# Performance work log

Measured on AMD Instinct MI355X. Metric: run time of the kernel, lower is better.

## Reference

```python
import jax, jax.numpy as jnp
import numpy as np

B, L_IN, C_IN, C_SKIP, C_OUT, DEPTH = 8, 512, 512, 512, 512, 4
D_INNER, D_STATE, D_CONV, DT_RANK = 1024, 16, 4, 32
EPS = 1e-5


def rmsnorm(x, w):
    return x * jax.lax.rsqrt(jnp.mean(x * x, axis=-1, keepdims=True) + EPS) * w


def layernorm(x, w, b):
    m = jnp.mean(x, axis=-1, keepdims=True)
    v = jnp.mean((x - m) ** 2, axis=-1, keepdims=True)
    return (x - m) * jax.lax.rsqrt(v + EPS) * w + b


def selective_scan(u, dt, A, Bm, Cm, Dp):
    # u, dt: (B, L, Di); A: (Di, N); Bm, Cm: (B, L, N); Dp: (Di,)
    def step(h, inp):
        dt_t, B_t, C_t, u_t = inp  # (B,Di),(B,N),(B,N),(B,Di)
        dA = jnp.exp(dt_t[..., None] * A)            # (B,Di,N)
        h = dA * h + (dt_t * u_t)[..., None] * B_t[:, None, :]
        y = jnp.einsum('bdn,bn->bd', h, C_t)
        return h, y

    Bb, L, Di = u.shape
    h0 = jnp.zeros((Bb, Di, A.shape[1]), u.dtype)
    xs = (dt.transpose(1, 0, 2), Bm.transpose(1, 0, 2),
          Cm.transpose(1, 0, 2), u.transpose(1, 0, 2))
    _, ys = jax.lax.scan(step, h0, xs)               # ys: (L,B,Di)
    return ys.transpose(1, 0, 2) + u * Dp


def mamba_block(x, in_w, cw, cb, xp_w, dtw, dtb, A_log, Dp, ow, ob):
    xz = x @ in_w.T                                   # (B,L,2*Di)
    xc, z = jnp.split(xz, 2, axis=-1)
    # causal depthwise conv, kernel D_CONV
    xc_t = jax.lax.conv_general_dilated(
        xc.transpose(0, 2, 1), cw[:, None, :], (1,), [(D_CONV - 1, 0)],
        feature_group_count=D_INNER,
        dimension_numbers=('NCH', 'OIH', 'NCH'))
    xc = jax.nn.silu((xc_t + cb[None, :, None]).transpose(0, 2, 1))
    xdbc = xc @ xp_w.T                                # (B,L,DT_RANK+2N)
    dtp = xdbc[..., :DT_RANK]
    Bm = xdbc[..., DT_RANK:DT_RANK + D_STATE]
    Cm = xdbc[..., DT_RANK + D_STATE:]
    dt = jax.nn.softplus(dtp @ dtw.T + dtb)
    A = -jnp.exp(A_log)
    y = selective_scan(xc, dt, A, Bm, Cm, Dp)
    return (y * jax.nn.silu(z)) @ ow.T + ob


def forward(motion_input, skip_feats, embed, w_up, b_up, w1, b1, rms_w, w2, b2,
            ln_w, ln_b, in_proj_w, conv_w, conv_b, x_proj_w, dt_proj_w,
            dt_proj_b, A_log, D_param, out_proj_w, out_proj_b,
            norm_f_w, norm_f_b):
    Bb, Lin, C = motion_input.shape
    # ConvTranspose1d(C, C, kernel=2, stride=2): non-overlapping expansion
    up = jnp.einsum('blc,cok->blko', motion_input, w_up)
    up = up.reshape(Bb, Lin * 2, C) + b_up            # (B, 2L, C)
    x = jnp.concatenate([up, skip_feats], axis=-1)    # (B, 2L, C+skip)
    # MLP: Linear -> RMSNorm -> SiLU -> Linear
    x = jax.nn.silu(rmsnorm(x @ w1.T + b1, rms_w)) @ w2.T + b2
    # MotionMamba: add embed, depth residual mamba blocks, final norm
    x = x + embed[:, None, :]
    for i in range(DEPTH):
        x = x + mamba_block(layernorm(x, ln_w[i], ln_b[i]), in_proj_w[i],
                            conv_w[i], conv_b[i], x_proj_w[i], dt_proj_w[i],
                            dt_proj_b[i], A_log[i], D_param[i],
                            out_proj_w[i], out_proj_b[i])
    return layernorm(x, norm_f_w, norm_f_b)


def setup_inputs():
    key = jax.random.key(0)
    ks = jax.random.split(key, 16)
    f = lambda k, sh: jax.random.normal(k, sh, jnp.float32) * 0.02
    inp = {}
    inp['motion_input'] = jax.random.normal(ks[0], (B, L_IN, C_IN), jnp.float32)
    inp['skip_feats'] = jax.random.normal(ks[1], (B, 2 * L_IN, C_SKIP), jnp.float32)
    inp['embed'] = jax.random.normal(ks[2], (B, C_OUT), jnp.float32)
    inp['w_up'] = f(ks[3], (C_IN, C_IN, 2))
    inp['b_up'] = jnp.zeros((C_IN,), jnp.float32)
    inp['w1'] = f(ks[4], (C_OUT, C_IN + C_SKIP))
    inp['b1'] = jnp.zeros((C_OUT,), jnp.float32)
    inp['rms_w'] = jnp.ones((C_OUT,), jnp.float32)
    inp['w2'] = f(ks[5], (C_OUT, C_OUT))
    inp['b2'] = jnp.zeros((C_OUT,), jnp.float32)
    inp['ln_w'] = jnp.ones((DEPTH, C_OUT), jnp.float32)
    inp['ln_b'] = jnp.zeros((DEPTH, C_OUT), jnp.float32)
    inp['in_proj_w'] = f(ks[6], (DEPTH, 2 * D_INNER, C_OUT))
    inp['conv_w'] = f(ks[7], (DEPTH, D_INNER, D_CONV))
    inp['conv_b'] = jnp.zeros((DEPTH, D_INNER), jnp.float32)
    inp['x_proj_w'] = f(ks[8], (DEPTH, DT_RANK + 2 * D_STATE, D_INNER))
    inp['dt_proj_w'] = f(ks[9], (DEPTH, D_INNER, DT_RANK))
    inp['dt_proj_b'] = jnp.full((DEPTH, D_INNER), -4.0, jnp.float32)
    inp['A_log'] = jnp.log(jnp.tile(jnp.arange(1, D_STATE + 1, dtype=jnp.float32), (DEPTH, D_INNER, 1)))
    inp['D_param'] = jnp.ones((DEPTH, D_INNER), jnp.float32)
    inp['out_proj_w'] = f(ks[10], (DEPTH, C_OUT, D_INNER))
    inp['out_proj_b'] = jnp.zeros((DEPTH, C_OUT), jnp.float32)
    inp['norm_f_w'] = jnp.ones((C_OUT,), jnp.float32)
    inp['norm_f_b'] = jnp.zeros((C_OUT,), jnp.float32)
    return inp


def reference(motion_input, skip_feats, embed, w_up, b_up, w1, b1, rms_w, w2,
              b2, ln_w, ln_b, in_proj_w, conv_w, conv_b, x_proj_w, dt_proj_w,
              dt_proj_b, A_log, D_param, out_proj_w, out_proj_b,
              norm_f_w, norm_f_b):
    return forward(motion_input, skip_feats, embed, w_up, b_up, w1, b1, rms_w,
                   w2, b2, ln_w, ln_b, in_proj_w, conv_w, conv_b, x_proj_w,
                   dt_proj_w, dt_proj_b, A_log, D_param, out_proj_w,
                   out_proj_b, norm_f_w, norm_f_b)
```

## Files before the change

kernel.cpp:

```cpp
#include <hip/hip_runtime.h>
#include <cstdint>
#include <cstddef>

#define DEV_INLINE __device__ __forceinline__

static constexpr float EPS = 1e-5f;

DEV_INLINE float sigmoidf_(float x) { return 1.0f / (1.0f + __expf(-x)); }
DEV_INLINE float siluf_(float x) { return x * sigmoidf_(x); }
DEV_INLINE float softplus_fast(float x) {
    return fmaxf(x, 0.0f) + __logf(1.0f + __expf(-fabsf(x)));
}
DEV_INLINE unsigned short f2bf(float x) {
    unsigned u = __builtin_bit_cast(unsigned, x);
    u += 0x7FFFu + ((u >> 16) & 1u);
    return (unsigned short)(u >> 16);
}
DEV_INLINE float bf2f(unsigned short s) {
    unsigned u = ((unsigned)s) << 16;
    return __builtin_bit_cast(float, u);
}

typedef __attribute__((ext_vector_type(8))) short bf16x8;
typedef __attribute__((ext_vector_type(4))) float f32x4;

DEV_INLINE void gload16(const unsigned short* src, char* ldsdst) {
    __builtin_amdgcn_global_load_lds(
        (const __attribute__((address_space(1))) unsigned int*)src,
        (__attribute__((address_space(3))) unsigned int*)ldsdst, 16, 0, 0);
}

DEV_INLINE void cvt8(const float* __restrict__ s, unsigned short* __restrict__ d, int t) {
    float4 f0 = *(const float4*)(s + (size_t)t * 8);
    float4 f1 = *(const float4*)(s + (size_t)t * 8 + 4);
    union { unsigned short u[8]; uint4 v; } pk;
    pk.u[0] = f2bf(f0.x); pk.u[1] = f2bf(f0.y); pk.u[2] = f2bf(f0.z); pk.u[3] = f2bf(f0.w);
    pk.u[4] = f2bf(f1.x); pk.u[5] = f2bf(f1.y); pk.u[6] = f2bf(f1.z); pk.u[7] = f2bf(f1.w);
    *(uint4*)(d + (size_t)t * 8) = pk.v;
}

__global__ __launch_bounds__(256) void prep_all(
    const float* __restrict__ motion, const float* __restrict__ wup,
    const float* __restrict__ w1, const float* __restrict__ w2,
    const float* __restrict__ in_proj_w, const float* __restrict__ out_proj_w,
    const float* __restrict__ x_proj_w, const float* __restrict__ dt_proj_w,
    const float* __restrict__ skip,
    unsigned short* __restrict__ mbf, unsigned short* __restrict__ wupT,
    unsigned short* __restrict__ w1b, unsigned short* __restrict__ w2b,
    unsigned short* __restrict__ lw, unsigned short* __restrict__ x0)
{
    int bid = (int)blockIdx.x, tid = (int)threadIdx.x;
    if (bid < 1024) {
        cvt8(motion, mbf, bid * 256 + tid);
    } else if (bid < 2048) {
        int t = (bid - 1024) * 256 + tid;
        int c = t >> 9, o = t & 511;
        float2 v = *(const float2*)(wup + (size_t)t * 2);
        wupT[(size_t)o * 512 + c] = f2bf(v.x);
        wupT[262144 + (size_t)o * 512 + c] = f2bf(v.y);
    } else if (bid < 2304) {
        cvt8(w1, w1b, (bid - 2048) * 256 + tid);
    } else if (bid < 2432) {
        cvt8(w2, w2b, (bid - 2304) * 256 + tid);
    } else if (bid < 5696) {
        int r = bid - 2432;
        int layer = r / 816;
        int lb = r - layer * 816;
        unsigned short* base = lw + (size_t)layer * 1671168;
        if (lb < 512) {
            cvt8(in_proj_w + (size_t)layer * 1048576, base, lb * 256 + tid);
        } else if (lb < 768) {
            cvt8(out_proj_w + (size_t)layer * 524288, base + 1048576,
                 (lb - 512) * 256 + tid);
        } else if (lb < 800) {
            cvt8(x_proj_w + (size_t)layer * 65536, base + 1572864,
                 (lb - 768) * 256 + tid);
        } else {
            cvt8(dt_proj_w + (size_t)layer * 32768, base + 1638400,
                 (lb - 800) * 256 + tid);
        }
    } else {
        int t = (bid - 5696) * 256 + tid;
        int row = t >> 6;
        int c8 = (t & 63) << 3;
        const float* s = skip + (size_t)row * 512 + c8;
        float4 f0 = *(const float4*)s;
        float4 f1 = *(const float4*)(s + 4);
        union { unsigned short u[8]; uint4 v; } pk;
        pk.u[0] = f2bf(f0.x); pk.u[1] = f2bf(f0.y); pk.u[2] = f2bf(f0.z); pk.u[3] = f2bf(f0.w);
        pk.u[4] = f2bf(f1.x); pk.u[5] = f2bf(f1.y); pk.u[6] = f2bf(f1.z); pk.u[7] = f2bf(f1.w);
        *(uint4*)(x0 + (size_t)row * 1024 + 512 + c8) = pk.v;
    }
}

template <int ACT, bool ACC, bool EMBED, bool OBF>
__global__ __launch_bounds__(256) void gemm_mfma(
    const unsigned short* __restrict__ A, int lda,
    const unsigned short* __restrict__ W, int ldw,
    void* __restrict__ Cv, int ldc, int N, int K, int gx,
    const float* __restrict__ bias, const float* __restrict__ embed)
{
    __shared__ unsigned short Asm[2][128 * 64];
    __shared__ unsigned short Wsm[2][128 * 64];
    const int tid = (int)threadIdx.x;
    const int lane = tid & 63;
    const int wv = tid >> 6;
    const int wm = wv >> 1, wn = wv & 1;

    const int nwg = (int)gridDim.x;
    const int lin = (int)blockIdx.x;
    const int logical = (lin & 7) * (nwg >> 3) + (lin >> 3);
    const int by = logical / gx;
    const int bx = logical - by * gx;
    const int bm = by * 128, bn = bx * 128;

    f32x4 acc[4][4] = {};
    const int l8 = lane >> 3;
    const int wc = lane & 7;
    const int wcg = wc ^ l8;
    const int NT = K >> 6;

    {
        char* aB = (char*)Asm[0];
        char* bB = (char*)Wsm[0];
#pragma unroll
        for (int i = 0; i < 4; ++i) {
            int rb = (i * 4 + wv) * 8;
            gload16(W + (size_t)(bn + rb + l8) * ldw + wcg * 8, bB + rb * 128);
            gload16(A + (size_t)(bm + rb + l8) * lda + wcg * 8, aB + rb * 128);
        }
    }

    for (int t = 0; t < NT; ++t) {
        const int cur = t & 1;
        if (t + 1 < NT) {
            const int k1 = (t + 1) << 6;
            char* aB = (char*)Asm[cur ^ 1];
            char* bB = (char*)Wsm[cur ^ 1];
#pragma unroll
            for (int i = 0; i < 4; ++i) {
                int rb = (i * 4 + wv) * 8;
                gload16(W + (size_t)(bn + rb + l8) * ldw + k1 + wcg * 8, bB + rb * 128);
                gload16(A + (size_t)(bm + rb + l8) * lda + k1 + wcg * 8, aB + rb * 128);
            }
            asm volatile("s_waitcnt vmcnt(8)" ::: "memory");
        } else {
            asm volatile("s_waitcnt vmcnt(0)" ::: "memory");
        }
        __builtin_amdgcn_s_barrier();
        __builtin_amdgcn_sched_barrier(0);

        const char* aB = (const char*)Asm[cur];
        const char* bB = (const char*)Wsm[cur];
        const int rA = wm * 64 + (lane & 15);
        const int rB = wn * 64 + (lane & 15);
        const int q = lane >> 4;
#pragma unroll
        for (int kk = 0; kk < 2; ++kk) {
            bf16x8 af[4], bfr[4];
#pragma unroll
            for (int mi = 0; mi < 4; ++mi) {
                int row = rA + mi * 16;
                int ch = (kk * 4 + q) ^ (row & 7);
                af[mi] = *(const bf16x8*)(aB + row * 128 + ch * 16);
            }
#pragma unroll
            for (int ni = 0; ni < 4; ++ni) {
                int row = rB + ni * 16;
                int ch = (kk * 4 + q) ^ (row & 7);
                bfr[ni] = *(const bf16x8*)(bB + row * 128 + ch * 16);
            }
#pragma unroll
            for (int mi = 0; mi < 4; ++mi)
#pragma unroll
                for (int ni = 0; ni < 4; ++ni)
                    acc[mi][ni] = __builtin_amdgcn_mfma_f32_16x16x32_bf16(
                        af[mi], bfr[ni], acc[mi][ni], 0, 0, 0);
        }
        asm volatile("" ::: "memory");
        __builtin_amdgcn_s_barrier();
        __builtin_amdgcn_sched_barrier(0);
    }

    const int cn = lane & 15;
    const int r0 = (lane >> 4) * 4;
    const int eb = EMBED ? (bm >> 10) * N : 0;
#pragma unroll
    for (int ni = 0; ni < 4; ++ni) {
        int col = bn + wn * 64 + ni * 16 + cn;
        float add = bias ? bias[col] : 0.0f;
        if (EMBED) add += embed[eb + col];
#pragma unroll
        for (int mi = 0; mi < 4; ++mi) {
#pragma unroll
            for (int r = 0; r < 4; ++r) {
                int row = bm + wm * 64 + mi * 16 + r0 + r;
                float v = acc[mi][ni][r] + add;
                if (ACT == 1) v = softplus_fast(v);
                if (OBF) {
                    ((unsigned short*)Cv)[(size_t)row * ldc + col] = f2bf(v);
                } else {
                    float* p = (float*)Cv + (size_t)row * ldc + col;
                    if (ACC) *p += v; else *p = v;
                }
            }
        }
    }
}

template <int ACT, bool ACC, bool EMBED, bool OBF, bool UPS>
__global__ __launch_bounds__(256) void gemm_mfma64(
    const unsigned short* __restrict__ A, int lda,
    const unsigned short* __restrict__ W, int ldw,
    void* __restrict__ Cv, int ldc, int N, int K, int gx,
    const float* __restrict__ bias, const float* __restrict__ embed)
{
    __shared__ unsigned short Asm[2][64 * 64];
    __shared__ unsigned short Wsm[2][64 * 64];
    const int tid = (int)threadIdx.x;
    const int lane = tid & 63;
    const int wv = tid >> 6;
    const int wm = wv >> 1, wn = wv & 1;

    const int nwg = (int)gridDim.x;
    const int lin = (int)blockIdx.x;
    const int logical = (lin & 7) * (nwg >> 3) + (lin >> 3);
    const int by = logical / gx;
    const int bx = logical - by * gx;
    const int bm = by * 64, bn = bx * 64;

    f32x4 acc[2][2] = {};
    const int l8 = lane >> 3;
    const int wc = lane & 7;
    const int wcg = wc ^ l8;
    const int NT = K >> 6;

    {
        char* aB = (char*)Asm[0];
        char* bB = (char*)Wsm[0];
#pragma unroll
        for (int i = 0; i < 2; ++i) {
            int rb = (i * 4 + wv) * 8;
            gload16(W + (size_t)(bn + rb + l8) * ldw + wcg * 8, bB + rb * 128);
            gload16(A + (size_t)(bm + rb + l8) * lda + wcg * 8, aB + rb * 128);
        }
    }

    for (int t = 0; t < NT; ++t) {
        const int cur = t & 1;
        if (t + 1 < NT) {
            const int k1 = (t + 1) << 6;
            char* aB = (char*)Asm[cur ^ 1];
            char* bB = (char*)Wsm[cur ^ 1];
#pragma unroll
            for (int i = 0; i < 2; ++i) {
                int rb = (i * 4 + wv) * 8;
                gload16(W + (size_t)(bn + rb + l8) * ldw + k1 + wcg * 8, bB + rb * 128);
                gload16(A + (size_t)(bm + rb + l8) * lda + k1 + wcg * 8, aB + rb * 128);
            }
            asm volatile("s_waitcnt vmcnt(4)" ::: "memory");
        } else {
            asm volatile("s_waitcnt vmcnt(0)" ::: "memory");
        }
        __builtin_amdgcn_s_barrier();
        __builtin_amdgcn_sched_barrier(0);

        const char* aB = (const char*)Asm[cur];
        const char* bB = (const char*)Wsm[cur];
        const int rA = wm * 32 + (lane & 15);
        const int rB = wn * 32 + (lane & 15);
        const int q = lane >> 4;
#pragma unroll
        for (int kk = 0; kk < 2; ++kk) {
            bf16x8 af[2], bfr[2];
#pragma unroll
            for (int mi = 0; mi < 2; ++mi) {
                int row = rA + mi * 16;
                int ch = (kk * 4 + q) ^ (row & 7);
                af[mi] = *(const bf16x8*)(aB + row * 128 + ch * 16);
            }
#pragma unroll
            for (int ni = 0; ni < 2; ++ni) {
                int row = rB + ni * 16;
                int ch = (kk * 4 + q) ^ (row & 7);
                bfr[ni] = *(const bf16x8*)(bB + row * 128 + ch * 16);
            }
#pragma unroll
            for (int mi = 0; mi < 2; ++mi)
#pragma unroll
                for (int ni = 0; ni < 2; ++ni)
                    acc[mi][ni] = __builtin_amdgcn_mfma_f32_16x16x32_bf16(
                        af[mi], bfr[ni], acc[mi][ni], 0, 0, 0);
        }
        asm volatile("" ::: "memory");
        __builtin_amdgcn_s_barrier();
        __builtin_amdgcn_sched_barrier(0);
    }

    const int cn = lane & 15;
    const int r0 = (lane >> 4) * 4;
    const int eb = EMBED ? (bm >> 10) * N : 0;
#pragma unroll
    for (int ni = 0; ni < 2; ++ni) {
        int col = bn + wn * 32 + ni * 16 + cn;
        float add = bias ? bias[UPS ? (col & 511) : col] : 0.0f;
        if (EMBED) add += embed[eb + col];
#pragma unroll
        for (int mi = 0; mi < 2; ++mi) {
#pragma unroll
            for (int r = 0; r < 4; ++r) {
                int row = bm + wm * 32 + mi * 16 + r0 + r;
                float v = acc[mi][ni][r] + add;
                if (ACT == 1) v = softplus_fast(v);
                if (UPS) {
                    size_t ad = (size_t)row * 2048 + ((col >> 9) << 10) + (col & 511);
                    ((unsigned short*)Cv)[ad] = f2bf(v);
                } else if (OBF) {
                    ((unsigned short*)Cv)[(size_t)row * ldc + col] = f2bf(v);
                } else {
                    float* p = (float*)Cv + (size_t)row * ldc + col;
                    if (ACC) *p += v; else *p = v;
                }
            }
        }
    }
}

__global__ __launch_bounds__(256) void gemm_dt(
    const unsigned short* __restrict__ xdbc,
    const unsigned short* __restrict__ wdt,
    const float* __restrict__ bias,
    unsigned short* __restrict__ out)
{
    __shared__ unsigned short S[128 * 136];
    const int tid = (int)threadIdx.x;
    const int lane = tid & 63;
    const int wv = tid >> 6;
    const int wm = wv >> 1, wn = wv & 1;

    const int lin = (int)blockIdx.x;
    const int logical = (lin & 7) * 64 + (lin >> 3);
    const int bm = (logical >> 3) * 128;
    const int bn = (logical & 7) * 128;

    const int fr = lane & 15;
    const int q = lane >> 4;

    bf16x8 af[4], wf[4];
#pragma unroll
    for (int mi = 0; mi < 4; ++mi)
        af[mi] = *(const bf16x8*)(xdbc + (size_t)(bm + wm * 64 + mi * 16 + fr) * 64 + q * 8);
#pragma unroll
    for (int ni = 0; ni < 4; ++ni)
        wf[ni] = *(const bf16x8*)(wdt + (size_t)(bn + wn * 64 + ni * 16 + fr) * 32 + q * 8);

    f32x4 acc[4][4] = {};
#pragma unroll
    for (int mi = 0; mi < 4; ++mi)
#pragma unroll
        for (int ni = 0; ni < 4; ++ni)
            acc[mi][ni] = __builtin_amdgcn_mfma_f32_16x16x32_bf16(
                af[mi], wf[ni], acc[mi][ni], 0, 0, 0);

    const int cn = lane & 15;
    const int r0 = (lane >> 4) * 4;
#pragma unroll
    for (int ni = 0; ni < 4; ++ni) {
        int lcol = wn * 64 + ni * 16 + cn;
        float add = bias[bn + lcol];
#pragma unroll
        for (int mi = 0; mi < 4; ++mi) {
#pragma unroll
            for (int r = 0; r < 4; ++r) {
                int lrow = wm * 64 + mi * 16 + r0 + r;
                S[lrow * 136 + lcol] = f2bf(softplus_fast(acc[mi][ni][r] + add));
            }
        }
    }
    __syncthreads();

    const int row = tid >> 1;
    const int half = tid & 1;
    const unsigned short* src = S + row * 136 + half * 64;
    unsigned short* dst = out + (size_t)(bm + row) * 1024 + bn + half * 64;
#pragma unroll
    for (int k = 0; k < 8; ++k) {
        uint4 v = *(const uint4*)(src + k * 8);
        *(uint4*)(dst + k * 8) = v;
    }
}

__global__ __launch_bounds__(128) void gemm_xdbc(
    const unsigned short* __restrict__ A,
    const unsigned short* __restrict__ W,
    unsigned short* __restrict__ C)
{
    __shared__ unsigned short Asm[64 * 64];
    __shared__ unsigned short Wsm[64 * 64];
    const int tid = (int)threadIdx.x;
    const int lane = tid & 63;
    const int w = tid >> 6;
    const int bm = blockIdx.x * 64;
    const int l8 = lane >> 3, wc = lane & 7, wcg = wc ^ l8;
    char* aB = (char*)Asm;
    char* bB = (char*)Wsm;

    f32x4 acc[2][4] = {};

    for (int k0 = 0; k0 < 1024; k0 += 64) {
#pragma unroll
        for (int i = 0; i < 4; ++i) {
            int rb = (i * 2 + w) * 8;
            gload16(A + (size_t)(bm + rb + l8) * 1024 + k0 + wcg * 8, aB + rb * 128);
            gload16(W + (size_t)(rb + l8) * 1024 + k0 + wcg * 8, bB + rb * 128);
        }
        __syncthreads();
        const int rA = w * 32 + (lane & 15);
        const int rB = (lane & 15);
        const int q = lane >> 4;
#pragma unroll
        for (int kk = 0; kk < 2; ++kk) {
            bf16x8 af[2], bfr[4];
#pragma unroll
            for (int mi = 0; mi < 2; ++mi) {
                int row = rA + mi * 16;
                int ch = (kk * 4 + q) ^ (row & 7);
                af[mi] = *(const bf16x8*)(aB + row * 128 + ch * 16);
            }
#pragma unroll
            for (int ni = 0; ni < 4; ++ni) {
                int row = rB + ni * 16;
                int ch = (kk * 4 + q) ^ (row & 7);
                bfr[ni] = *(const bf16x8*)(bB + row * 128 + ch * 16);
            }
#pragma unroll
            for (int mi = 0; mi < 2; ++mi)
#pragma unroll
                for (int ni = 0; ni < 4; ++ni)
                    acc[mi][ni] = __builtin_amdgcn_mfma_f32_16x16x32_bf16(
                        af[mi], bfr[ni], acc[mi][ni], 0, 0, 0);
        }
        __syncthreads();
    }
    const int cn = lane & 15;
    const int r0 = (lane >> 4) * 4;
#pragma unroll
    for (int mi = 0; mi < 2; ++mi)
#pragma unroll
        for (int ni = 0; ni < 4; ++ni)
#pragma unroll
            for (int r = 0; r < 4; ++r) {
                int row = bm + w * 32 + mi * 16 + r0 + r;
                C[(size_t)row * 64 + ni * 16 + cn] = f2bf(acc[mi][ni][r]);
            }
}

template <bool BFOUT>
__global__ __launch_bounds__(256) void layernorm_k(
    const float* __restrict__ x, void* __restrict__ outp,
    const float* __restrict__ w, const float* __restrict__ b)
{
    const int row = blockIdx.x * 4 + ((int)threadIdx.x >> 6);
    const int lane = (int)threadIdx.x & 63;
    const float* xr = x + (size_t)row * 512;
    float4 v0 = *(const float4*)(xr + lane * 4);
    float4 v1 = *(const float4*)(xr + 256 + lane * 4);
    float s = v0.x + v0.y + v0.z + v0.w + v1.x + v1.y + v1.z + v1.w;
    float q = v0.x*v0.x + v0.y*v0.y + v0.z*v0.z + v0.w*v0.w
            + v1.x*v1.x + v1.y*v1.y + v1.z*v1.z + v1.w*v1.w;
#pragma unroll
    for (int o = 32; o; o >>= 1) {
        s += __shfl_xor(s, o, 64);
        q += __shfl_xor(q, o, 64);
    }
    const float mean = s * (1.0f / 512.0f);
    const float var = q * (1.0f / 512.0f) - mean * mean;
    const float rstd = rsqrtf(var + EPS);
    float4 w0 = *(const float4*)(w + lane * 4);
    float4 w1 = *(const float4*)(w + 256 + lane * 4);
    float4 b0 = *(const float4*)(b + lane * 4);
    float4 b1 = *(const float4*)(b + 256 + lane * 4);
    float4 o0, o1;
    o0.x = (v0.x - mean) * rstd * w0.x + b0.x;
    o0.y = (v0.y - mean) * rstd * w0.y + b0.y;
    o0.z = (v0.z - mean) * rstd * w0.z + b0.z;
    o0.w = (v0.w - mean) * rstd * w0.w + b0.w;
    o1.x = (v1.x - mean) * rstd * w1.x + b1.x;
    o1.y = (v1.y - mean) * rstd * w1.y + b1.y;
    o1.z = (v1.z - mean) * rstd * w1.z + b1.z;
    o1.w = (v1.w - mean) * rstd * w1.w + b1.w;
    if (BFOUT) {
        unsigned short* ob = (unsigned short*)outp + (size_t)row * 512;
        union { unsigned short u[4]; uint2 v; } p0, p1;
        p0.u[0] = f2bf(o0.x); p0.u[1] = f2bf(o0.y); p0.u[2] = f2bf(o0.z); p0.u[3] = f2bf(o0.w);
        p1.u[0] = f2bf(o1.x); p1.u[1] = f2bf(o1.y); p1.u[2] = f2bf(o1.z); p1.u[3] = f2bf(o1.w);
        *(uint2*)(ob + lane * 4) = p0.v;
        *(uint2*)(ob + 256 + lane * 4) = p1.v;
    } else {
        float* orow = (float*)outp + (size_t)row * 512;
        *(float4*)(orow + lane * 4) = o0;
        *(float4*)(orow + 256 + lane * 4) = o1;
    }
}

__global__ __launch_bounds__(256) void rms_silu_k(
    const float* __restrict__ x, unsigned short* __restrict__ o,
    const float* __restrict__ w)
{
    const int row = blockIdx.x * 4 + ((int)threadIdx.x >> 6);
    const int lane = (int)threadIdx.x & 63;
    const float* xr = x + (size_t)row * 512;
    float4 v0 = *(const float4*)(xr + lane * 4);
    float4 v1 = *(const float4*)(xr + 256 + lane * 4);
    float q = v0.x*v0.x + v0.y*v0.y + v0.z*v0.z + v0.w*v0.w
            + v1.x*v1.x + v1.y*v1.y + v1.z*v1.z + v1.w*v1.w;
#pragma unroll
    for (int of = 32; of; of >>= 1) q += __shfl_xor(q, of, 64);
    const float scale = rsqrtf(q * (1.0f / 512.0f) + EPS);
    float4 w0 = *(const float4*)(w + lane * 4);
    float4 w1 = *(const float4*)(w + 256 + lane * 4);
    union { unsigned short u[4]; uint2 v; } p0, p1;
    p0.u[0] = f2bf(siluf_(v0.x * scale * w0.x));
    p0.u[1] = f2bf(siluf_(v0.y * scale * w0.y));
    p0.u[2] = f2bf(siluf_(v0.z * scale * w0.z));
    p0.u[3] = f2bf(siluf_(v0.w * scale * w0.w));
    p1.u[0] = f2bf(siluf_(v1.x * scale * w1.x));
    p1.u[1] = f2bf(siluf_(v1.y * scale * w1.y));
    p1.u[2] = f2bf(siluf_(v1.z * scale * w1.z));
    p1.u[3] = f2bf(siluf_(v1.w * scale * w1.w));
    unsigned short* ob = o + (size_t)row * 512;
    *(uint2*)(ob + lane * 4) = p0.v;
    *(uint2*)(ob + 256 + lane * 4) = p1.v;
}

__global__ __launch_bounds__(256) void conv_silu_k2(
    const unsigned short* __restrict__ xz, unsigned short* __restrict__ ub,
    const float* __restrict__ cw, const float* __restrict__ cb)
{
    int t = blockIdx.x * 256 + (int)threadIdx.x;
    int d = t & 1023;
    int bc = t >> 10;
    int b = bc >> 4, ch = bc & 15;
    int l0 = ch * 64;
    float4 w4 = *(const float4*)(cw + (size_t)d * 4);
    float bias = cb[d];
    const unsigned short* src = xz + ((size_t)(b * 1024 + l0)) * 2048 + d;
    unsigned short* dst = ub + ((size_t)(b * 1024 + l0)) * 1024 + d;
    float x0 = 0.f, x1 = 0.f, x2 = 0.f;
    if (l0 > 0) {
        x0 = bf2f(src[-(size_t)3 * 2048]);
        x1 = bf2f(src[-(size_t)2 * 2048]);
        x2 = bf2f(src[-(size_t)1 * 2048]);
    }
    for (int l = 0; l < 64; ++l) {
        float x3 = bf2f(src[(size_t)l * 2048]);
        float v = fmaf(x0, w4.x, fmaf(x1, w4.y, fmaf(x2, w4.z, fmaf(x3, w4.w, bias))));
        dst[(size_t)l * 1024] = f2bf(siluf_(v));
        x0 = x1; x1 = x2; x2 = x3;
    }
}

template <int CTRL>
DEV_INLINE float dpp_f(float x) {
    int yi = __builtin_amdgcn_update_dpp(
        0, __builtin_bit_cast(int, x), CTRL, 0xF, 0xF, true);
    return __builtin_bit_cast(float, yi);
}

template <int PHASE>
__global__ __launch_bounds__(128) void scan7(
    const unsigned short* __restrict__ dtp,
    const unsigned short* ubf,
    unsigned short* ybf,
    const unsigned short* __restrict__ xdbc,
    const unsigned short* __restrict__ zbf,
    float* __restrict__ hp,
    const float* __restrict__ A_log,
    const float* __restrict__ Dp)
{
    __shared__ float SDT[32 * 70];
    __shared__ float SB[32][20];
    __shared__ float SC[PHASE == 2 ? 32 : 1][20];
    __shared__ float YS[PHASE == 2 ? 32 : 1][36];

    const int lin = (int)blockIdx.x;
    const int logical = (lin & 7) * 256 + (lin >> 3);
    const int g = logical & 31;
    const int r = logical >> 5;
    const int c = r & 7, b = r >> 3;
    if (PHASE == 1 && c == 7) return;
    const int tid = (int)threadIdx.x;
    const int dl = tid >> 2, qq = tid & 3;
    const int dblk = g << 5;
    const int d = dblk + dl;
    const int m0 = b * 1024 + c * 128;

    float An[4];
#pragma unroll
    for (int j = 0; j < 4; ++j)
        An[j] = -__expf(A_log[(size_t)d * 16 + qq * 4 + j]);

    float h[4] = {};
    float prod[4] = {1.f, 1.f, 1.f, 1.f};
    if (PHASE == 2) {
        const float* hpb = hp + ((size_t)(b * 1024 + d)) * 256 + qq * 8;
        for (int cc = 0; cc < c; ++cc) {
            float4 v0 = *(const float4*)(hpb + cc * 32);
            float4 v1 = *(const float4*)(hpb + cc * 32 + 4);
            h[0] = fmaf(v0.y, h[0], v0.x);
            h[1] = fmaf(v0.w, h[1], v0.z);
            h[2] = fmaf(v1.y, h[2], v1.x);
            h[3] = fmaf(v1.w, h[3], v1.z);
        }
    }

    const int sr = tid >> 3;
    const int sg = (tid & 7) * 4;
    const int bcr = tid >> 2;
    const int bne = (tid & 3) << 2;

    uint2 rd0, rd1, ru0, ru1, rB, rC;

    {
        size_t ra = (size_t)(m0 + sr);
        size_t rb2 = (size_t)(m0 + 16 + sr);
        rd0 = *(const uint2*)(dtp + ra * 1024 + dblk + sg);
        rd1 = *(const uint2*)(dtp + rb2 * 1024 + dblk + sg);
        ru0 = *(const uint2*)(ubf + ra * 1024 + dblk + sg);
        ru1 = *(const uint2*)(ubf + rb2 * 1024 + dblk + sg);
        rB = *(const uint2*)(xdbc + (size_t)(m0 + bcr) * 64 + 32 + bne);
        if (PHASE == 2)
            rC = *(const uint2*)(xdbc + (size_t)(m0 + bcr) * 64 + 48 + bne);
    }

    for (int s = 0; s < 4; ++s) {
        const int lbase = s * 32;
        if (PHASE == 1 && s > 0) __syncthreads();
        {
            const unsigned short* dp0 = (const unsigned short*)&rd0;
            const unsigned short* dp1 = (const unsigned short*)&rd1;
            const unsigned short* up0 = (const unsigned short*)&ru0;
            const unsigned short* up1 = (const unsigned short*)&ru1;
            const int l20 = sr >> 1, hh = (sr & 1) * 2;
            const int l21 = (16 + sr) >> 1;
#pragma unroll
            for (int j = 0; j < 4; ++j) {
                float d0 = bf2f(dp0[j]);
                float2 v0 = {d0, d0 * bf2f(up0[j])};
                *(float2*)&SDT[(sg + j) * 70 + l20 * 4 + hh] = v0;
                float d1 = bf2f(dp1[j]);
                float2 v1 = {d1, d1 * bf2f(up1[j])};
                *(float2*)&SDT[(sg + j) * 70 + l21 * 4 + hh] = v1;
            }
            const unsigned short* bb = (const unsigned short*)&rB;
            float4 bv = {bf2f(bb[0]), bf2f(bb[1]), bf2f(bb[2]), bf2f(bb[3])};
            *(float4*)&SB[bcr][bne] = bv;
            if (PHASE == 2) {
                const unsigned short* cp = (const unsigned short*)&rC;
                float4 cv = {bf2f(cp[0]), bf2f(cp[1]), bf2f(cp[2]), bf2f(cp[3])};
                *(float4*)&SC[bcr][bne] = cv;
            }
        }
        if (s < 3) {
            const int nb = lbase + 32;
            size_t ra = (size_t)(m0 + nb + sr);
            size_t rb2 = (size_t)(m0 + nb + 16 + sr);
            rd0 = *(const uint2*)(dtp + ra * 1024 + dblk + sg);
            rd1 = *(const uint2*)(dtp + rb2 * 1024 + dblk + sg);
            ru0 = *(const uint2*)(ubf + ra * 1024 + dblk + sg);
            ru1 = *(const uint2*)(ubf + rb2 * 1024 + dblk + sg);
            rB = *(const uint2*)(xdbc + (size_t)(m0 + nb + bcr) * 64 + 32 + bne);
            if (PHASE == 2)
                rC = *(const uint2*)(xdbc + (size_t)(m0 + nb + bcr) * 64 + 48 + bne);
        }
        __syncthreads();

        for (int l2 = 0; l2 < 16; ++l2) {
            float4 sd = *(const float4*)&SDT[dl * 70 + l2 * 4];
            float4 B0 = *(const float4*)&SB[2 * l2][qq * 4];
            float4 B1 = *(const float4*)&SB[2 * l2 + 1][qq * 4];
            float p0 = 0.0f, p1 = 0.0f;
            float4 C0, C1;
            if (PHASE == 2) {
                C0 = *(const float4*)&SC[2 * l2][qq * 4];
                C1 = *(const float4*)&SC[2 * l2 + 1][qq * 4];
            }
            const float* B0p = (const float*)&B0;
            const float* B1p = (const float*)&B1;
            const float* C0p = (const float*)&C0;
            const float* C1p = (const float*)&C1;
#pragma unroll
            for (int j = 0; j < 4; ++j) {
                float e0 = __expf(sd.x * An[j]);
                if (PHASE == 1) prod[j] *= e0;
                h[j] = fmaf(e0, h[j], sd.y * B0p[j]);
                if (PHASE == 2) p0 = fmaf(h[j], C0p[j], p0);
                float e1 = __expf(sd.z * An[j]);
                if (PHASE == 1) prod[j] *= e1;
                h[j] = fmaf(e1, h[j], sd.w * B1p[j]);
                if (PHASE == 2) p1 = fmaf(h[j], C1p[j], p1);
            }
            if (PHASE == 2) {
                p0 += dpp_f<0xB1>(p0);
                p0 += dpp_f<0x4E>(p0);
                p1 += dpp_f<0xB1>(p1);
                p1 += dpp_f<0x4E>(p1);
                if (qq == 0) {
                    YS[2 * l2][dl] = p0;
                    YS[2 * l2 + 1][dl] = p1;
                }
            }
        }

        if (PHASE == 2) {
            __syncthreads();
            const int row = tid >> 2;
            const int d8 = (tid & 3) * 8;
            size_t gr = (size_t)(m0 + lbase + row);
            float4 p40 = *(const float4*)&YS[row][d8];
            float4 p41 = *(const float4*)&YS[row][d8 + 4];
            uint4 uu = *(const uint4*)(ubf + gr * 1024 + dblk + d8);
            uint4 zz = *(const uint4*)(zbf + gr * 2048 + 1024 + dblk + d8);
            float4 D0 = *(const float4*)(Dp + dblk + d8);
            float4 D1 = *(const float4*)(Dp + dblk + d8 + 4);
            const unsigned short* up = (const unsigned short*)&uu;
            const unsigned short* zp = (const unsigned short*)&zz;
            const float* pp0 = (const float*)&p40;
            const float* pp1 = (const float*)&p41;
            const float* dd0 = (const float*)&D0;
            const float* dd1 = (const float*)&D1;
            union { unsigned short u[8]; uint4 v; } pk;
#pragma unroll
            for (int j = 0; j < 4; ++j) {
                float y = fmaf(bf2f(up[j]), dd0[j], pp0[j]) * siluf_(bf2f(zp[j]));
                pk.u[j] = f2bf(y);
            }
#pragma unroll
            for (int j = 0; j < 4; ++j) {
                float y = fmaf(bf2f(up[4 + j]), dd1[j], pp1[j]) * siluf_(bf2f(zp[4 + j]));
                pk.u[4 + j] = f2bf(y);
            }
            __syncthreads();
            *(uint4*)(ybf + gr * 1024 + dblk + d8) = pk.v;
        }
    }

    if (PHASE == 1) {
        float* hpo = hp + ((size_t)(b * 1024 + d)) * 256 + c * 32 + qq * 8;
        float4 o0 = {h[0], prod[0], h[1], prod[1]};
        float4 o1 = {h[2], prod[2], h[3], prod[3]};
        *(float4*)hpo = o0;
        *(float4*)(hpo + 4) = o1;
    }
}

extern "C" void kernel_launch(void* const* d_in, const int* in_sizes, int n_in,
                              void* d_out, int out_size, void* d_ws, size_t ws_size,
                              hipStream_t stream)
{
    const float* motion     = (const float*)d_in[0];
    const float* skip       = (const float*)d_in[1];
    const float* embed      = (const float*)d_in[2];
    const float* w_up       = (const float*)d_in[3];
    const float* b_up       = (const float*)d_in[4];
    const float* w1         = (const float*)d_in[5];
    const float* b1         = (const float*)d_in[6];
    const float* rms_w      = (const float*)d_in[7];
    const float* w2         = (const float*)d_in[8];
    const float* b2         = (const float*)d_in[9];
    const float* ln_w       = (const float*)d_in[10];
    const float* ln_b       = (const float*)d_in[11];
    const float* in_proj_w  = (const float*)d_in[12];
    const float* conv_w     = (const float*)d_in[13];
    const float* conv_b     = (const float*)d_in[14];
    const float* x_proj_w   = (const float*)d_in[15];
    const float* dt_proj_w  = (const float*)d_in[16];
    const float* dt_proj_b  = (const float*)d_in[17];
    const float* A_log      = (const float*)d_in[18];
    const float* D_param    = (const float*)d_in[19];
    const float* out_proj_w = (const float*)d_in[20];
    const float* out_proj_b = (const float*)d_in[21];
    const float* norm_f_w   = (const float*)d_in[22];
    const float* norm_f_b   = (const float*)d_in[23];
    float* out = (float*)d_out;
    float* ws = (float*)d_ws;

    float* xbuf = ws;
    float* xlnf = ws + 4194304;
    unsigned short* xzbf  = (unsigned short*)(ws + 8388608);
    unsigned short* ubf   = (unsigned short*)(ws + 16777216);
    unsigned short* dtybf = (unsigned short*)(ws + 20971520);
    unsigned short* xdbc  = (unsigned short*)(ws + 25165824);
    float* hp  = ws + 25427968;
    unsigned short* xsbf = (unsigned short*)(ws + 29622272);
    unsigned short* mbf  = (unsigned short*)(ws + 31719424);
    unsigned short* wupT = (unsigned short*)(ws + 32768000);
    unsigned short* w1b  = (unsigned short*)(ws + 33030144);
    unsigned short* w2b  = (unsigned short*)(ws + 33292288);
    unsigned short* lw   = (unsigned short*)(ws + 33423360);

    unsigned short* x0bf = xzbf;

    dim3 blk(256);

    prep_all<<<dim3(7744), blk, 0, stream>>>(
        motion, w_up, w1, w2, in_proj_w, out_proj_w, x_proj_w, dt_proj_w,
        skip, mbf, wupT, w1b, w2b, lw, x0bf);

    gemm_mfma64<0, false, false, true, true><<<dim3(1024), blk, 0, stream>>>(
        mbf, 512, wupT, 512, x0bf, 0, 1024, 512, 16, b_up, nullptr);

    gemm_mfma64<0, false, false, false, false><<<dim3(1024), blk, 0, stream>>>(
        x0bf, 1024, w1b, 1024, xlnf, 512, 512, 1024, 8, b1, nullptr);
    rms_silu_k<<<dim3(2048), blk, 0, stream>>>(xlnf, xsbf, rms_w);

    gemm_mfma64<0, false, true, false, false><<<dim3(1024), blk, 0, stream>>>(
        xsbf, 512, w2b, 512, xbuf, 512, 512, 512, 8, b2, embed);

    for (int i = 0; i < 4; ++i) {
        unsigned short* ipw = lw + (size_t)i * 1671168;
        unsigned short* opw = ipw + 1048576;
        unsigned short* xpw = ipw + 1572864;
        unsigned short* wdt = ipw + 1638400;
        layernorm_k<true><<<dim3(2048), blk, 0, stream>>>(
            xbuf, xsbf, ln_w + (size_t)i * 512, ln_b + (size_t)i * 512);
        gemm_mfma<0, false, false, true><<<dim3(1024), blk, 0, stream>>>(
            xsbf, 512, ipw, 512, xzbf, 2048, 2048, 512, 16, nullptr, nullptr);
        conv_silu_k2<<<dim3(512), blk, 0, stream>>>(
            xzbf, ubf, conv_w + (size_t)i * 4096, conv_b + (size_t)i * 1024);
        gemm_xdbc<<<dim3(128), dim3(128), 0, stream>>>(ubf, xpw, xdbc);
        gemm_dt<<<dim3(512), blk, 0, stream>>>(
            xdbc, wdt, dt_proj_b + (size_t)i * 1024, dtybf);
        scan7<1><<<dim3(2048), dim3(128), 0, stream>>>(
            dtybf, ubf, nullptr, xdbc, xzbf, hp,
            A_log + (size_t)i * 16384, D_param + (size_t)i * 1024);
        scan7<2><<<dim3(2048), dim3(128), 0, stream>>>(
            dtybf, ubf, ubf, xdbc, xzbf, hp,
            A_log + (size_t)i * 16384, D_param + (size_t)i * 1024);
        gemm_mfma64<0, true, false, false, false><<<dim3(1024), blk, 0, stream>>>(
            ubf, 1024, opw, 1024, xbuf, 512, 512, 1024, 8,
            out_proj_b + (size_t)i * 512, nullptr);
    }

    layernorm_k<false><<<dim3(2048), blk, 0, stream>>>(xbuf, out, norm_f_w, norm_f_b);
}
```

Before: 691.4 us.

## Store scan staging tiles in LDS as bf16 and prefetch epilogue u/z operands

The chunked selective-scan kernel now keeps dt, dt*u, B and C in shared memory as packed bf16 instead of fp32. Each inner iteration reads one 16-byte vector covering four timesteps, which cuts LDS footprint and the number of LDS loads. The u, z and D operands for the output epilogue are prefetched into registers one chunk ahead, and the barrier placement is reorganised. The trade-off is that dt*u is rounded to bf16 before use, and the extra bf16-to-fp32 conversions add ALU work and slightly reduce accuracy.

After: 747.8 us. +8.2%, slower.

```diff
diff --git a/kernel.cpp b/kernel.cpp
--- a/kernel.cpp
+++ b/kernel.cpp
@@ -22,6 +22,7 @@
 }
 
 typedef __attribute__((ext_vector_type(8))) short bf16x8;
+typedef __attribute__((ext_vector_type(8))) unsigned short u16x8;
 typedef __attribute__((ext_vector_type(4))) float f32x4;
 
 DEV_INLINE void gload16(const unsigned short* src, char* ldsdst) {
@@ -568,7 +569,7 @@
 }
 
 template <int PHASE>
-__global__ __launch_bounds__(128) void scan7(
+__global__ __launch_bounds__(128) void scan8(
     const unsigned short* __restrict__ dtp,
     const unsigned short* ubf,
     unsigned short* ybf,
@@ -578,9 +579,9 @@
     const float* __restrict__ A_log,
     const float* __restrict__ Dp)
 {
-    __shared__ float SDT[32 * 70];
-    __shared__ float SB[32][20];
-    __shared__ float SC[PHASE == 2 ? 32 : 1][20];
+    __shared__ unsigned short SDTb[32][18][4];
+    __shared__ unsigned short BB[16][4][8];
+    __shared__ unsigned short CCb[PHASE == 2 ? 16 : 1][4][8];
     __shared__ float YS[PHASE == 2 ? 32 : 1][36];
 
     const int lin = (int)blockIdx.x;
@@ -614,121 +615,109 @@
         }
     }
 
-    const int sr = tid >> 3;
+    const int sr2 = tid >> 3;
     const int sg = (tid & 7) * 4;
     const int bcr = tid >> 2;
     const int bne = (tid & 3) << 2;
+    const int yrow = tid >> 2;
+    const int yd8 = (tid & 3) * 8;
 
     uint2 rd0, rd1, ru0, ru1, rB, rC;
+    uint4 pu, pz, npu, npz;
+    float4 pD0, pD1;
 
     {
-        size_t ra = (size_t)(m0 + sr);
-        size_t rb2 = (size_t)(m0 + 16 + sr);
+        size_t ra = (size_t)(m0 + 2 * sr2);
         rd0 = *(const uint2*)(dtp + ra * 1024 + dblk + sg);
-        rd1 = *(const uint2*)(dtp + rb2 * 1024 + dblk + sg);
+        rd1 = *(const uint2*)(dtp + (ra + 1) * 1024 + dblk + sg);
         ru0 = *(const uint2*)(ubf + ra * 1024 + dblk + sg);
-        ru1 = *(const uint2*)(ubf + rb2 * 1024 + dblk + sg);
+        ru1 = *(const uint2*)(ubf + (ra + 1) * 1024 + dblk + sg);
         rB = *(const uint2*)(xdbc + (size_t)(m0 + bcr) * 64 + 32 + bne);
-        if (PHASE == 2)
+        if (PHASE == 2) {
             rC = *(const uint2*)(xdbc + (size_t)(m0 + bcr) * 64 + 48 + bne);
+            pu = *(const uint4*)(ubf + (size_t)(m0 + yrow) * 1024 + dblk + yd8);
+            pz = *(const uint4*)(zbf + (size_t)(m0 + yrow) * 2048 + 1024 + dblk + yd8);
+            pD0 = *(const float4*)(Dp + dblk + yd8);
+            pD1 = *(const float4*)(Dp + dblk + yd8 + 4);
+        }
     }
 
     for (int s = 0; s < 4; ++s) {
         const int lbase = s * 32;
-        if (PHASE == 1 && s > 0) __syncthreads();
         {
             const unsigned short* dp0 = (const unsigned short*)&rd0;
             const unsigned short* dp1 = (const unsigned short*)&rd1;
             const unsigned short* up0 = (const unsigned short*)&ru0;
             const unsigned short* up1 = (const unsigned short*)&ru1;
-            const int l20 = sr >> 1, hh = (sr & 1) * 2;
-            const int l21 = (16 + sr) >> 1;
 #pragma unroll
             for (int j = 0; j < 4; ++j) {
-                float d0 = bf2f(dp0[j]);
-                float2 v0 = {d0, d0 * bf2f(up0[j])};
-                *(float2*)&SDT[(sg + j) * 70 + l20 * 4 + hh] = v0;
-                float d1 = bf2f(dp1[j]);
-                float2 v1 = {d1, d1 * bf2f(up1[j])};
-                *(float2*)&SDT[(sg + j) * 70 + l21 * 4 + hh] = v1;
-            }
-            const unsigned short* bb = (const unsigned short*)&rB;
-            float4 bv = {bf2f(bb[0]), bf2f(bb[1]), bf2f(bb[2]), bf2f(bb[3])};
-            *(float4*)&SB[bcr][bne] = bv;
-            if (PHASE == 2) {
-                const unsigned short* cp = (const unsigned short*)&rC;
-                float4 cv = {bf2f(cp[0]), bf2f(cp[1]), bf2f(cp[2]), bf2f(cp[3])};
-                *(float4*)&SC[bcr][bne] = cv;
-            }
+                float dt0 = bf2f(dp0[j]), dt1 = bf2f(dp1[j]);
+                union { unsigned short u[4]; uint2 v; } pk;
+                pk.u[0] = dp0[j];
+                pk.u[1] = f2bf(dt0 * bf2f(up0[j]));
+                pk.u[2] = dp1[j];
+                pk.u[3] = f2bf(dt1 * bf2f(up1[j]));
+                *(uint2*)&SDTb[sg + j][sr2][0] = pk.v;
+            }
+            *(uint2*)&BB[bcr >> 1][bne >> 2][(bcr & 1) * 4] = rB;
+            if (PHASE == 2)
+                *(uint2*)&CCb[bcr >> 1][bne >> 2][(bcr & 1) * 4] = rC;
         }
         if (s < 3) {
             const int nb = lbase + 32;
-            size_t ra = (size_t)(m0 + nb + sr);
-            size_t rb2 = (size_t)(m0 + nb + 16 + sr);
+            size_t ra = (size_t)(m0 + nb + 2 * sr2);
             rd0 = *(const uint2*)(dtp + ra * 1024 + dblk + sg);
-            rd1 = *(const uint2*)(dtp + rb2 * 1024 + dblk + sg);
+            rd1 = *(const uint2*)(dtp + (ra + 1) * 1024 + dblk + sg);
             ru0 = *(const uint2*)(ubf + ra * 1024 + dblk + sg);
-            ru1 = *(const uint2*)(ubf + rb2 * 1024 + dblk + sg);
+            ru1 = *(const uint2*)(ubf + (ra + 1) * 1024 + dblk + sg);
             rB = *(const uint2*)(xdbc + (size_t)(m0 + nb + bcr) * 64 + 32 + bne);
-            if (PHASE == 2)
+            if (PHASE == 2) {
                 rC = *(const uint2*)(xdbc + (size_t)(m0 + nb + bcr) * 64 + 48 + bne);
+                npu = *(const uint4*)(ubf + (size_t)(m0 + nb + yrow) * 1024 + dblk + yd8);
+                npz = *(const uint4*)(zbf + (size_t)(m0 + nb + yrow) * 2048 + 1024 + dblk + yd8);
+            }
         }
         __syncthreads();
 
-        for (int l2 = 0; l2 < 16; ++l2) {
-            float4 sd = *(const float4*)&SDT[dl * 70 + l2 * 4];
-            float4 B0 = *(const float4*)&SB[2 * l2][qq * 4];
-            float4 B1 = *(const float4*)&SB[2 * l2 + 1][qq * 4];
-            float p0 = 0.0f, p1 = 0.0f;
-            float4 C0, C1;
+        for (int l4 = 0; l4 < 8; ++l4) {
+            u16x8 sdp = *(const u16x8*)&SDTb[dl][l4 * 2][0];
+            unsigned short bs[16], cs[16];
+            *(u16x8*)&bs[0] = *(const u16x8*)&BB[2 * l4][qq][0];
+            *(u16x8*)&bs[8] = *(const u16x8*)&BB[2 * l4 + 1][qq][0];
             if (PHASE == 2) {
-                C0 = *(const float4*)&SC[2 * l2][qq * 4];
-                C1 = *(const float4*)&SC[2 * l2 + 1][qq * 4];
-            }
-            const float* B0p = (const float*)&B0;
-            const float* B1p = (const float*)&B1;
-            const float* C0p = (const float*)&C0;
-            const float* C1p = (const float*)&C1;
-#pragma unroll
-            for (int j = 0; j < 4; ++j) {
-                float e0 = __expf(sd.x * An[j]);
-                if (PHASE == 1) prod[j] *= e0;
-                h[j] = fmaf(e0, h[j], sd.y * B0p[j]);
-                if (PHASE == 2) p0 = fmaf(h[j], C0p[j], p0);
-                float e1 = __expf(sd.z * An[j]);
-                if (PHASE == 1) prod[j] *= e1;
-                h[j] = fmaf(e1, h[j], sd.w * B1p[j]);
-                if (PHASE == 2) p1 = fmaf(h[j], C1p[j], p1);
-            }
-            if (PHASE == 2) {
-                p0 += dpp_f<0xB1>(p0);
-                p0 += dpp_f<0x4E>(p0);
-                p1 += dpp_f<0xB1>(p1);
-                p1 += dpp_f<0x4E>(p1);
-                if (qq == 0) {
-                    YS[2 * l2][dl] = p0;
-                    YS[2 * l2 + 1][dl] = p1;
+                *(u16x8*)&cs[0] = *(const u16x8*)&CCb[2 * l4][qq][0];
+                *(u16x8*)&cs[8] = *(const u16x8*)&CCb[2 * l4 + 1][qq][0];
+            }
+#pragma unroll
+            for (int t = 0; t < 4; ++t) {
+                float dtR = bf2f(sdp[2 * t]);
+                float dtuR = bf2f(sdp[2 * t + 1]);
+                float p = 0.0f;
+#pragma unroll
+                for (int j = 0; j < 4; ++j) {
+                    float e = __expf(dtR * An[j]);
+                    if (PHASE == 1) prod[j] *= e;
+                    h[j] = fmaf(e, h[j], dtuR * bf2f(bs[4 * t + j]));
+                    if (PHASE == 2) p = fmaf(h[j], bf2f(cs[4 * t + j]), p);
+                }
+                if (PHASE == 2) {
+                    p += dpp_f<0xB1>(p);
+                    p += dpp_f<0x4E>(p);
+                    if (qq == 0) YS[l4 * 4 + t][dl] = p;
                 }
             }
         }
 
         if (PHASE == 2) {
             __syncthreads();
-            const int row = tid >> 2;
-            const int d8 = (tid & 3) * 8;
-            size_t gr = (size_t)(m0 + lbase + row);
-            float4 p40 = *(const float4*)&YS[row][d8];
-            float4 p41 = *(const float4*)&YS[row][d8 + 4];
-            uint4 uu = *(const uint4*)(ubf + gr * 1024 + dblk + d8);
-            uint4 zz = *(const uint4*)(zbf + gr * 2048 + 1024 + dblk + d8);
-            float4 D0 = *(const float4*)(Dp + dblk + d8);
-            float4 D1 = *(const float4*)(Dp + dblk + d8 + 4);
-            const unsigned short* up = (const unsigned short*)&uu;
-            const unsigned short* zp = (const unsigned short*)&zz;
+            float4 p40 = *(const float4*)&YS[yrow][yd8];
+            float4 p41 = *(const float4*)&YS[yrow][yd8 + 4];
+            const unsigned short* up = (const unsigned short*)&pu;
+            const unsigned short* zp = (const unsigned short*)&pz;
             const float* pp0 = (const float*)&p40;
             const float* pp1 = (const float*)&p41;
-            const float* dd0 = (const float*)&D0;
-            const float* dd1 = (const float*)&D1;
+            const float* dd0 = (const float*)&pD0;
+            const float* dd1 = (const float*)&pD1;
             union { unsigned short u[8]; uint4 v; } pk;
 #pragma unroll
             for (int j = 0; j < 4; ++j) {
@@ -740,9 +729,10 @@
                 float y = fmaf(bf2f(up[4 + j]), dd1[j], pp1[j]) * siluf_(bf2f(zp[4 + j]));
                 pk.u[4 + j] = f2bf(y);
             }
-            __syncthreads();
-            *(uint4*)(ybf + gr * 1024 + dblk + d8) = pk.v;
-        }
+            *(uint4*)(ybf + (size_t)(m0 + lbase + yrow) * 1024 + dblk + yd8) = pk.v;
+            if (s < 3) { pu = npu; pz = npz; }
+        }
+        __syncthreads();
     }
 
     if (PHASE == 1) {
@@ -831,10 +821,10 @@
         gemm_xdbc<<<dim3(128), dim3(128), 0, stream>>>(ubf, xpw, xdbc);
         gemm_dt<<<dim3(512), blk, 0, stream>>>(
             xdbc, wdt, dt_proj_b + (size_t)i * 1024, dtybf);
-        scan7<1><<<dim3(2048), dim3(128), 0, stream>>>(
+        scan8<1><<<dim3(2048), dim3(128), 0, stream>>>(
             dtybf, ubf, nullptr, xdbc, xzbf, hp,
             A_log + (size_t)i * 16384, D_param + (size_t)i * 1024);
-        scan7<2><<<dim3(2048), dim3(128), 0, stream>>>(
+        scan8<2><<<dim3(2048), dim3(128), 0, stream>>>(
             dtybf, ubf, ubf, xdbc, xzbf, hp,
             A_log + (size_t)i * 16384, D_param + (size_t)i * 1024);
         gemm_mfma64<0, true, false, false, false><<<dim3(1024), blk, 0, stream>>>(
```
